# Optimization experiments

Hardware: AMD Instinct MI355X
Metric: run time of the kernel (lower is better)

Reference implementation:

```python
import jax, jax.numpy as jnp
import numpy as np

BATCH, SEQLEN, D_MODEL, D_STATE, D_FF = 16, 8192, 256, 256, 1024
RMIN, RMAX, MAX_PHASE = 0.0, 1.0, 2.0 * np.pi


def setup_inputs() -> dict:
    key = jax.random.key(0)
    ks = jax.random.split(key, 12)
    x = jax.random.normal(ks[0], (BATCH, SEQLEN, D_MODEL), jnp.float32)
    # LRU stable exponential parameterization (Orvieto et al.)
    u1 = jax.random.uniform(ks[1], (D_STATE,), jnp.float32)
    u2 = jax.random.uniform(ks[2], (D_STATE,), jnp.float32)
    nu_log = jnp.log(-0.5 * jnp.log(u1 * (RMAX**2 - RMIN**2) + RMIN**2))
    theta_log = jnp.log(MAX_PHASE * u2)
    lam_abs = jnp.exp(-jnp.exp(nu_log))
    gamma_log = 0.5 * jnp.log(1.0 - lam_abs**2)
    B_re = jax.random.normal(ks[3], (D_STATE, D_MODEL), jnp.float32) / np.sqrt(2.0 * D_MODEL)
    B_im = jax.random.normal(ks[4], (D_STATE, D_MODEL), jnp.float32) / np.sqrt(2.0 * D_MODEL)
    C_re = jax.random.normal(ks[5], (D_MODEL, D_STATE), jnp.float32) / np.sqrt(D_STATE)
    C_im = jax.random.normal(ks[6], (D_MODEL, D_STATE), jnp.float32) / np.sqrt(D_STATE)
    D = jax.random.normal(ks[7], (D_MODEL, D_MODEL), jnp.float32) / np.sqrt(D_MODEL)
    W_fc = jax.random.normal(ks[8], (D_MODEL, D_FF), jnp.float32) / np.sqrt(D_MODEL)
    b_fc = jnp.zeros((D_FF,), jnp.float32)
    W_proj = jax.random.normal(ks[9], (D_FF, D_MODEL), jnp.float32) / np.sqrt(D_FF)
    b_proj = jnp.zeros((D_MODEL,), jnp.float32)
    return dict(x=x, nu_log=nu_log, theta_log=theta_log, gamma_log=gamma_log,
                B_re=B_re, B_im=B_im, C_re=C_re, C_im=C_im, D=D,
                W_fc=W_fc, b_fc=b_fc, W_proj=W_proj, b_proj=b_proj)


def _lru_scan(x, nu_log, theta_log, gamma_log, B_re, B_im, C_re, C_im, D):
    # diagonal complex recurrence: s_t = lam * s_{t-1} + gamma * B @ u_t ; y_t = Re(C s_t) + D u_t
    lam = jnp.exp(-jnp.exp(nu_log)) * jnp.exp(1j * jnp.exp(theta_log))      # (S,) complex
    Bn = (B_re + 1j * B_im) * jnp.exp(gamma_log)[:, None]                   # (S, D)
    Bu = jnp.einsum('bld,sd->bls', x + 0j, Bn)                              # (B, L, S) complex
    lam_b = jnp.broadcast_to(lam, Bu.shape)

    def comb(a, b):
        a_l, a_s = a
        b_l, b_s = b
        return a_l * b_l, b_l * a_s + b_s

    _, states = jax.lax.associative_scan(comb, (lam_b, Bu), axis=1)
    C = C_re + 1j * C_im
    return jnp.einsum('bls,os->blo', states, C).real + x @ D.T


def reference(x, nu_log, theta_log, gamma_log, B_re, B_im, C_re, C_im, D,
              W_fc, b_fc, W_proj, b_proj):
    z = _lru_scan(x, nu_log, theta_log, gamma_log, B_re, B_im, C_re, C_im, D)
    # MLP (dropout=0 -> identity)
    h = jax.nn.gelu(z @ W_fc + b_fc, approximate=False)
    z = h @ W_proj + b_proj
    return z + x  # residual
```

## Files before the change

### kernel.cpp

```cpp
#include <hip/hip_runtime.h>
#include <hip/hip_bf16.h>
#include <math.h>

#define B_SZ 16
#define L_SZ 8192
#define DM   256
#define SS   256
#define FF   1024
#define M_SZ (B_SZ * L_SZ)
#define TCH  128
#define NCH  (L_SZ / TCH)

#define BM 128
#define BN 128
#define BK 32

typedef __bf16 bf16x8 __attribute__((ext_vector_type(8)));
typedef float  f32x4  __attribute__((ext_vector_type(4)));

__device__ __forceinline__ void gld_lds16(const __bf16* g, __bf16* l) {
  __builtin_amdgcn_global_load_lds(
      (const __attribute__((address_space(1))) unsigned int*)g,
      (__attribute__((address_space(3))) unsigned int*)l, 16, 0, 0);
}

__device__ __forceinline__ float gelu_exact_fast(float t) {
  const float at = fabsf(t);
  const float a  = at * 0.70710678118654752f;
  const float k  = __builtin_amdgcn_rcpf(fmaf(0.3275911f, a, 1.0f));
  float P = fmaf(1.061405429f, k, -1.453152027f);
  P = fmaf(P, k, 1.421413741f);
  P = fmaf(P, k, -0.284496736f);
  P = fmaf(P, k, 0.254829592f);
  P = P * k;
  const float e = __expf(-a * a);
  const float half_t  = 0.5f * t;
  const float half_at = 0.5f * at;
  return fmaf(-half_at, P * e, half_t + half_at);
}

__global__ void prep_kernel(const float* __restrict__ nu_log, const float* __restrict__ th_log,
                            const float* __restrict__ ga_log,
                            const float* __restrict__ B_re, const float* __restrict__ B_im,
                            const float* __restrict__ C_re, const float* __restrict__ C_im,
                            const float* __restrict__ Dmat,
                            const float* __restrict__ W_fc, const float* __restrict__ W_proj,
                            __bf16* __restrict__ Wb, __bf16* __restrict__ Wz,
                            __bf16* __restrict__ Wfc, __bf16* __restrict__ Wp,
                            float* __restrict__ lam)
{
  const int idx = blockIdx.x * 256 + threadIdx.x;
  if (idx < SS) {
    float la = expf(-expf(nu_log[idx]));
    float th = expf(th_log[idx]);
    lam[2*idx]   = la * cosf(th);
    lam[2*idx+1] = la * sinf(th);
  }
  if (idx < SS*DM) {
    int s = idx >> 8, d = idx & 255;
    float eg = expf(ga_log[s]);
    Wb[(size_t)(2*s)*DM + d]   = (__bf16)(B_re[idx] * eg);
    Wb[(size_t)(2*s+1)*DM + d] = (__bf16)(B_im[idx] * eg);
  }
  if (idx < DM*SS) {
    int o = idx >> 8, s = idx & 255;
    Wz[(size_t)o*768 + 2*s]     = (__bf16)( C_re[idx]);
    Wz[(size_t)o*768 + 2*s + 1] = (__bf16)(-C_im[idx]);
    Wz[(size_t)o*768 + 512 + s] = (__bf16)( Dmat[idx]);
  }
  if (idx < FF*DM) {
    int f = idx >> 8, d = idx & 255;
    Wfc[idx] = (__bf16)(W_fc[(size_t)d*FF + f]);
    int o = idx >> 10, f2 = idx & 1023;
    Wp[idx] = (__bf16)(W_proj[(size_t)f2*DM + o]);
  }
}

__global__ __launch_bounds__(256) void convert_x(const float* __restrict__ x, __bf16* __restrict__ S_all)
{
  const long i = ((long)blockIdx.x * 256 + threadIdx.x) * 4;
  float4 v = *(const float4*)(x + i);
  const long m = i >> 8;
  const int  d = (int)(i & 255);
  union { __bf16 h[4]; uint2 u; } pk;
  pk.h[0] = (__bf16)v.x; pk.h[1] = (__bf16)v.y; pk.h[2] = (__bf16)v.z; pk.h[3] = (__bf16)v.w;
  *(uint2*)(S_all + m*768 + 512 + d) = pk.u;
}

template<int K, int LDA, int LDC, int MODE, int NT>
__global__ __launch_bounds__(256, 2) void gemm_bt(const __bf16* __restrict__ A,
                                                  const __bf16* __restrict__ Bw,
                                                  void* __restrict__ Cout,
                                                  const float* __restrict__ bias,
                                                  const float* __restrict__ resid)
{
  __shared__ __attribute__((aligned(16))) __bf16 sA[BM * BK];
  __shared__ __attribute__((aligned(16))) __bf16 sB[BN * BK];

  const int tid  = threadIdx.x;
  const int lane = tid & 63;
  const int wave = tid >> 6;
  const int wm = (wave & 1) * 64;
  const int wn = (wave >> 1) * 64;

  constexpr int PER = 16 * NT;
  const int blk = blockIdx.x;
  const int sb  = blk / PER;
  const int rem = blk & (PER - 1);
  const long m0 = (long)((sb << 4) + (rem & 15)) * BM;
  const long n0 = (long)(rem >> 4) * BN;

  f32x4 acc[4][4] = {};

  const int r  = tid >> 2;
  const int c8 = (tid & 3) * 8;
  const __bf16* gA = A  + (m0 + r) * (long)LDA + c8;
  const __bf16* gB = Bw + (n0 + r) * (long)K   + c8;

  const int ar = lane & 15;
  const int ak = (lane >> 4) * 8;

  for (int k0 = 0; k0 < K; k0 += BK) {
    gld_lds16(gA,                  &sA[tid * 8]);
    gld_lds16(gA + 64 * (long)LDA, &sA[2048 + tid * 8]);
    gld_lds16(gB,                  &sB[tid * 8]);
    gld_lds16(gB + 64 * (long)K,   &sB[2048 + tid * 8]);
    gA += BK; gB += BK;
    __syncthreads();

    bf16x8 af[4], bg[4];
    #pragma unroll
    for (int i = 0; i < 4; ++i)
      af[i] = *(const bf16x8*)&sA[(wm + i * 16 + ar) * BK + ak];
    #pragma unroll
    for (int j = 0; j < 4; ++j)
      bg[j] = *(const bf16x8*)&sB[(wn + j * 16 + ar) * BK + ak];
    #pragma unroll
    for (int i = 0; i < 4; ++i)
      #pragma unroll
      for (int j = 0; j < 4; ++j)
        acc[i][j] = __builtin_amdgcn_mfma_f32_16x16x32_bf16(af[i], bg[j], acc[i][j], 0, 0, 0);
    __syncthreads();
  }

  const int col_l = lane & 15;
  const int row_l = (lane >> 4) * 4;
  #pragma unroll
  for (int i = 0; i < 4; ++i) {
    #pragma unroll
    for (int j = 0; j < 4; ++j) {
      const long row = m0 + wm + i * 16 + row_l;
      const long col = n0 + wn + j * 16 + col_l;
      #pragma unroll
      for (int rr = 0; rr < 4; ++rr) {
        const float v = acc[i][j][rr];
        const long idx = (row + rr) * (long)LDC + col;
        if constexpr (MODE == 1) {
          ((__bf16*)Cout)[idx] = (__bf16)v;
        } else if constexpr (MODE == 2) {
          const float t = v + bias[col];
          ((__bf16*)Cout)[idx] = (__bf16)gelu_exact_fast(t);
        } else {
          ((float*)Cout)[idx] = v + bias[col] + resid[idx];
        }
      }
    }
  }
}

#define CSTEP(vr, vi) { float nr_ = fmaf(lr, sr, fmaf(-li, si, (vr))); \
                        float ni_ = fmaf(lr, si, fmaf( li, sr, (vi))); sr = nr_; si = ni_; }

union bupk { unsigned int u; __bf16 h[2]; };

__global__ __launch_bounds__(256) void scan_carry(const __bf16* __restrict__ Bu,
                                                  const float* __restrict__ lam,
                                                  float2* __restrict__ carr)
{
  const int s  = threadIdx.x;
  const int bc = blockIdx.x;
  const float lr = lam[2*s], li = lam[2*s+1];
  const unsigned int* bu = (const unsigned int*)(Bu + (size_t)bc * (TCH * 512)) + s;
  float sr = 0.f, si = 0.f;
  bupk v0, v1, v2, v3;
  v0.u = bu[0]; v1.u = bu[256]; v2.u = bu[512]; v3.u = bu[768];
  for (int t = 0; t < TCH - 4; t += 4) {
    bupk n0, n1, n2, n3;
    n0.u = bu[(t+4)*256]; n1.u = bu[(t+5)*256]; n2.u = bu[(t+6)*256]; n3.u = bu[(t+7)*256];
    CSTEP((float)v0.h[0], (float)v0.h[1]); CSTEP((float)v1.h[0], (float)v1.h[1]);
    CSTEP((float)v2.h[0], (float)v2.h[1]); CSTEP((float)v3.h[0], (float)v3.h[1]);
    v0 = n0; v1 = n1; v2 = n2; v3 = n3;
  }
  CSTEP((float)v0.h[0], (float)v0.h[1]); CSTEP((float)v1.h[0], (float)v1.h[1]);
  CSTEP((float)v2.h[0], (float)v2.h[1]); CSTEP((float)v3.h[0], (float)v3.h[1]);
  carr[(size_t)bc * 256 + s] = make_float2(sr, si);
}

__global__ __launch_bounds__(256) void scan_prefix(const float2* __restrict__ carr,
                                                   const float* __restrict__ lam,
                                                   float2* __restrict__ pre)
{
  const int s = threadIdx.x;
  const int b = blockIdx.x;
  float ar = lam[2*s], ai = lam[2*s+1];
  #pragma unroll
  for (int i = 0; i < 7; ++i) { float nr = ar*ar - ai*ai, ni = 2.f*ar*ai; ar = nr; ai = ni; }
  float pr = 0.f, pi = 0.f;
  for (int c = 0; c < NCH; ++c) {
    const size_t off = (size_t)(b * NCH + c) * 256 + s;
    pre[off] = make_float2(pr, pi);
    float2 cv = carr[off];
    float nr = fmaf(ar, pr, fmaf(-ai, pi, cv.x));
    float ni = fmaf(ar, pi, fmaf( ai, pr, cv.y));
    pr = nr; pi = ni;
  }
}

__global__ __launch_bounds__(256) void scan_apply(const __bf16* __restrict__ Bu,
                                                  const float* __restrict__ lam,
                                                  const float2* __restrict__ pre,
                                                  __bf16* __restrict__ S_all)
{
  const int s  = threadIdx.x;
  const int bc = blockIdx.x;
  const float lr = lam[2*s], li = lam[2*s+1];
  float2 p = pre[(size_t)bc * 256 + s];
  float sr = p.x, si = p.y;
  const unsigned int* bu = (const unsigned int*)(Bu + (size_t)bc * (TCH * 512)) + s;
  __bf16* outp = S_all + (size_t)bc * (TCH * 768) + 2 * s;
  #define APSTEP(v, t) { CSTEP((float)(v).h[0], (float)(v).h[1]); \
    union { __bf16 h[2]; unsigned int u; } pk_; pk_.h[0] = (__bf16)sr; pk_.h[1] = (__bf16)si; \
    *(unsigned int*)(outp + (size_t)(t) * 768) = pk_.u; }
  bupk v0, v1, v2, v3;
  v0.u = bu[0]; v1.u = bu[256]; v2.u = bu[512]; v3.u = bu[768];
  for (int t = 0; t < TCH - 4; t += 4) {
    bupk n0, n1, n2, n3;
    n0.u = bu[(t+4)*256]; n1.u = bu[(t+5)*256]; n2.u = bu[(t+6)*256]; n3.u = bu[(t+7)*256];
    APSTEP(v0, t); APSTEP(v1, t+1); APSTEP(v2, t+2); APSTEP(v3, t+3);
    v0 = n0; v1 = n1; v2 = n2; v3 = n3;
  }
  { const int t = TCH - 4; APSTEP(v0, t); APSTEP(v1, t+1); APSTEP(v2, t+2); APSTEP(v3, t+3); }
  #undef APSTEP
}

extern "C" void kernel_launch(void* const* d_in, const int* in_sizes, int n_in,
                              void* d_out, int out_size, void* d_ws, size_t ws_size,
                              hipStream_t stream)
{
  const float* x      = (const float*)d_in[0];
  const float* nu_log = (const float*)d_in[1];
  const float* th_log = (const float*)d_in[2];
  const float* ga_log = (const float*)d_in[3];
  const float* B_re   = (const float*)d_in[4];
  const float* B_im   = (const float*)d_in[5];
  const float* C_re   = (const float*)d_in[6];
  const float* C_im   = (const float*)d_in[7];
  const float* Dmat   = (const float*)d_in[8];
  const float* W_fc   = (const float*)d_in[9];
  const float* b_fc   = (const float*)d_in[10];
  const float* W_proj = (const float*)d_in[11];
  const float* b_proj = (const float*)d_in[12];

  char* ws = (char*)d_ws;
  __bf16* S_all = (__bf16*)(ws);
  __bf16* Bu    = (__bf16*)(ws + 201326592);
  __bf16* Hbuf  = (__bf16*)(ws + 201326592);
  __bf16* Wb    = (__bf16*)(ws + 469762048);
  __bf16* Wz    = (__bf16*)(ws + 470024192);
  __bf16* Wfc   = (__bf16*)(ws + 470417408);
  __bf16* Wp    = (__bf16*)(ws + 470941696);
  float*  lam   = (float*) (ws + 471465984);
  if (ws_size < 471468032ULL) return;

  char* ob = (char*)d_out;
  __bf16* Zbuf = (__bf16*)ob;
  float2* carr = (float2*)(ob + 67108864);
  float2* pre  = (float2*)(ob + 69206016);

  prep_kernel<<<1024, 256, 0, stream>>>(nu_log, th_log, ga_log, B_re, B_im,
                                        C_re, C_im, Dmat, W_fc, W_proj,
                                        Wb, Wz, Wfc, Wp, lam);
  convert_x<<<M_SZ * DM / (256 * 4), 256, 0, stream>>>(x, S_all);

  gemm_bt<256, 768, 512, 1, 4><<<(M_SZ / BM) * 4, 256, 0, stream>>>(S_all + 512, Wb, Bu, nullptr, nullptr);

  scan_carry <<<B_SZ * NCH, 256, 0, stream>>>(Bu, lam, carr);
  scan_prefix<<<B_SZ,       256, 0, stream>>>(carr, lam, pre);
  scan_apply <<<B_SZ * NCH, 256, 0, stream>>>(Bu, lam, pre, S_all);

  gemm_bt<768, 768, 256, 1, 2><<<(M_SZ / BM) * 2, 256, 0, stream>>>(S_all, Wz, Zbuf, nullptr, nullptr);
  gemm_bt<256, 256, 1024, 2, 8><<<(M_SZ / BM) * 8, 256, 0, stream>>>(Zbuf, Wfc, Hbuf, b_fc, nullptr);
  gemm_bt<1024, 1024, 256, 3, 2><<<(M_SZ / BM) * 2, 256, 0, stream>>>(Hbuf, Wp, d_out, b_proj, x);
}
```

Baseline: 758.5 us.

## Multi-buffer GEMM LDS tiles with a prefetch depth of three

```diff
diff --git a/kernel.cpp b/kernel.cpp
--- a/kernel.cpp
+++ b/kernel.cpp
@@ -94,8 +94,7 @@
                                                   const float* __restrict__ bias,
                                                   const float* __restrict__ resid)
 {
-  __shared__ __attribute__((aligned(16))) __bf16 sA[BM * BK];
-  __shared__ __attribute__((aligned(16))) __bf16 sB[BN * BK];
+  __shared__ __attribute__((aligned(16))) __bf16 smem[32768];
 
   const int tid  = threadIdx.x;
   const int lane = tid & 63;
@@ -120,28 +119,47 @@
   const int ar = lane & 15;
   const int ak = (lane >> 4) * 8;
 
-  for (int k0 = 0; k0 < K; k0 += BK) {
-    gld_lds16(gA,                  &sA[tid * 8]);
-    gld_lds16(gA + 64 * (long)LDA, &sA[2048 + tid * 8]);
-    gld_lds16(gB,                  &sB[tid * 8]);
-    gld_lds16(gB + 64 * (long)K,   &sB[2048 + tid * 8]);
-    gA += BK; gB += BK;
-    __syncthreads();
+  constexpr int NK = K / BK;
+
+  #define STAGE(t, q) { \
+    const long ko_ = (long)(t) * BK; \
+    __bf16* sa_ = smem + (q) * 4096; \
+    __bf16* sb_ = smem + 16384 + (q) * 4096; \
+    gld_lds16(gA + ko_,                  &sa_[tid * 8]); \
+    gld_lds16(gA + ko_ + 64 * (long)LDA, &sa_[2048 + tid * 8]); \
+    gld_lds16(gB + ko_,                  &sb_[tid * 8]); \
+    gld_lds16(gB + ko_ + 64 * (long)K,   &sb_[2048 + tid * 8]); }
+
+  STAGE(0, 0);
+  STAGE(1, 1);
+  STAGE(2, 2);
+
+  #pragma unroll 4
+  for (int i = 0; i < NK; ++i) {
+    if (i < NK - 2)       { asm volatile("s_waitcnt vmcnt(8)" ::: "memory"); }
+    else if (i == NK - 2) { asm volatile("s_waitcnt vmcnt(4)" ::: "memory"); }
+    else                  { asm volatile("s_waitcnt vmcnt(0)" ::: "memory"); }
+    __builtin_amdgcn_s_barrier();
+
+    if (i + 3 < NK) STAGE(i + 3, (i + 3) & 3);
+
+    const __bf16* sAc = smem + (i & 3) * 4096;
+    const __bf16* sBc = smem + 16384 + (i & 3) * 4096;
 
     bf16x8 af[4], bg[4];
     #pragma unroll
-    for (int i = 0; i < 4; ++i)
-      af[i] = *(const bf16x8*)&sA[(wm + i * 16 + ar) * BK + ak];
+    for (int ii = 0; ii < 4; ++ii)
+      af[ii] = *(const bf16x8*)&sAc[(wm + ii * 16 + ar) * BK + ak];
     #pragma unroll
     for (int j = 0; j < 4; ++j)
-      bg[j] = *(const bf16x8*)&sB[(wn + j * 16 + ar) * BK + ak];
+      bg[j] = *(const bf16x8*)&sBc[(wn + j * 16 + ar) * BK + ak];
     #pragma unroll
-    for (int i = 0; i < 4; ++i)
+    for (int ii = 0; ii < 4; ++ii)
       #pragma unroll
       for (int j = 0; j < 4; ++j)
-        acc[i][j] = __builtin_amdgcn_mfma_f32_16x16x32_bf16(af[i], bg[j], acc[i][j], 0, 0, 0);
-    __syncthreads();
-  }
+        acc[ii][j] = __builtin_amdgcn_mfma_f32_16x16x32_bf16(af[ii], bg[j], acc[ii][j], 0, 0, 0);
+  }
+  #undef STAGE
 
   const int col_l = lane & 15;
   const int row_l = (lane >> 4) * 4;
```

Measured after the change: 783.8 us. 1.03x slower.
